# Kernel optimization log

Measured on AMD Instinct MI355X. Metric: run time of the kernel, lower is better.

The kernel has to match this reference:

```python
import jax, jax.numpy as jnp
import numpy as np

B, N, C = 4, 2048, 1024
H = 16
D = C // H

def setup_inputs() -> dict:
    key = jax.random.key(0)
    k1, k2, k3 = jax.random.split(key, 3)
    x = jax.random.normal(k1, (B, N, C), dtype=jnp.float32)
    qkv_w = jax.random.normal(k2, (3 * C, C), dtype=jnp.float32) * (1.0 / np.sqrt(C))
    qkv_b = jax.random.normal(k3, (3 * C,), dtype=jnp.float32) * 0.02
    return {"x": x, "qkv_w": qkv_w, "qkv_b": qkv_b}

def reference(x, qkv_w, qkv_b):
    b, n, c = x.shape
    # torch Linear: x @ W^T + b
    qkv = x @ qkv_w.T + qkv_b                      # [B,N,3C]
    qkv = qkv.reshape(b, n, 3, H, D)
    qkv = jnp.transpose(qkv, (2, 0, 3, 1, 4))       # [3,B,H,N,D]
    q, k, v = qkv[0], qkv[1], qkv[2]
    attn = jnp.einsum('bhnd,bhmd->bhnm', q, k) / jnp.sqrt(jnp.asarray(D, x.dtype))
    attn = jax.nn.softmax(attn, axis=-1)
    out = jnp.einsum('bhnm,bhmd->bhnd', attn, v)    # [B,H,N,D]
    out = jnp.transpose(out, (0, 2, 1, 3)).reshape(b, n, c)
    return out
```

## Files before the change

kernel.cpp:

```cpp
#include <hip/hip_runtime.h>
#include <hip/hip_bf16.h>

typedef __attribute__((ext_vector_type(8))) short short8;
typedef __attribute__((ext_vector_type(4))) float f32x4;
typedef __attribute__((ext_vector_type(4))) unsigned int u32x4;
typedef unsigned short u16;
typedef unsigned int u32;

typedef u32 __attribute__((address_space(1))) as1_u32;
typedef u32 __attribute__((address_space(3))) as3_u32;

#define NB 4
#define SEQ 2048
#define CH 1024
#define NH 16
#define HD 64
#define M_TOT (NB*SEQ)
#define N_TOT (3*CH)
#define K_TOT CH
#define SCL 0.18033688f

#define MFMA16(a,b,c) __builtin_amdgcn_mfma_f32_16x16x32_bf16((a),(b),(c),0,0,0)

__device__ __forceinline__ u16 f2bf(float f) {
    union { float f; u32 u; } v; v.f = f;
    u32 u = v.u;
    return (u16)((u + 0x7fffu + ((u >> 16) & 1u)) >> 16);
}

__device__ __forceinline__ u32 pkbf2(float a, float b) {
    union { __hip_bfloat162 h; u32 u; } x;
    x.h = __float22bfloat162_rn(float2{a, b});
    return x.u;
}

__global__ void cvt_bf16_kernel(const float* __restrict__ src, u16* __restrict__ dst, int n8) {
    int i = blockIdx.x * 256 + threadIdx.x;
    if (i >= n8) return;
    const float4* s4 = (const float4*)src;
    float4 a = s4[2*i], b = s4[2*i+1];
    u32x4 r;
    r[0] = pkbf2(a.x, a.y); r[1] = pkbf2(a.z, a.w);
    r[2] = pkbf2(b.x, b.y); r[3] = pkbf2(b.z, b.w);
    *(u32x4*)(dst + (size_t)i*8) = r;
}

__global__ __launch_bounds__(256) void qkv_gemm_kernel(
        const u16* __restrict__ A, const u16* __restrict__ W,
        const float* __restrict__ bias,
        u16* __restrict__ qw, u16* __restrict__ kw, u16* __restrict__ vtw)
{
    __shared__ u16 As[128*32];
    __shared__ u16 Bs[128*32];
    const int t = threadIdx.x;
    const int wave = t >> 6;
    const int lane = t & 63;
    const int l15 = lane & 15, lhi = lane >> 4;
    const int wr = wave >> 1, wc = wave & 1;
    const int bm = blockIdx.x, bn = blockIdx.y;

    f32x4 acc[4][4] = {};

    const int arow = t >> 2;
    const int acol = (t & 3) * 8;
    const u16* gA = A + (size_t)(bm*128 + arow)*K_TOT + acol;
    const u16* gB = W + (size_t)(bn*128 + arow)*K_TOT + acol;

    for (int k0 = 0; k0 < K_TOT; k0 += 32) {
        #pragma unroll
        for (int i = 0; i < 2; ++i) {
            __builtin_amdgcn_global_load_lds(
                (const as1_u32*)(gA + (size_t)i*64*K_TOT + k0),
                (as3_u32*)(As + i*2048 + wave*512), 16, 0, 0);
            __builtin_amdgcn_global_load_lds(
                (const as1_u32*)(gB + (size_t)i*64*K_TOT + k0),
                (as3_u32*)(Bs + i*2048 + wave*512), 16, 0, 0);
        }
        __syncthreads();
        short8 af[4], bfr[4];
        #pragma unroll
        for (int m = 0; m < 4; ++m)
            af[m] = *(const short8*)(As + (wr*64 + m*16 + l15)*32 + lhi*8);
        #pragma unroll
        for (int n = 0; n < 4; ++n)
            bfr[n] = *(const short8*)(Bs + (wc*64 + n*16 + l15)*32 + lhi*8);
        #pragma unroll
        for (int m = 0; m < 4; ++m)
            #pragma unroll
            for (int n = 0; n < 4; ++n)
                acc[m][n] = MFMA16(af[m], bfr[n], acc[m][n]);
        __syncthreads();
    }

    const int colbase = bn*128 + wc*64;
    const int which = colbase >> 10;
    float bv[4]; int hh[4], dd[4];
    #pragma unroll
    for (int n = 0; n < 4; ++n) {
        int cg = colbase + n*16 + l15;
        bv[n] = bias[cg];
        int hd = cg & 1023;
        hh[n] = hd >> 6; dd[n] = hd & 63;
    }
    #pragma unroll
    for (int m = 0; m < 4; ++m) {
        int rowg = bm*128 + wr*64 + m*16 + lhi*4;
        #pragma unroll
        for (int j = 0; j < 4; ++j) {
            int rg = rowg + j;
            int b = rg >> 11, nseq = rg & 2047;
            #pragma unroll
            for (int n = 0; n < 4; ++n) {
                float val = acc[m][n][j] + bv[n];
                size_t bhn = (size_t)(b*NH + hh[n]);
                if (which == 0) {
                    qw[(bhn*SEQ + nseq)*HD + dd[n]] = f2bf(val * SCL);
                } else if (which == 1) {
                    kw[(bhn*SEQ + nseq)*HD + dd[n]] = f2bf(val);
                } else {
                    vtw[(bhn*HD + dd[n])*SEQ + nseq] = f2bf(val);
                }
            }
        }
    }
}

__global__ __launch_bounds__(512, 4) void attn_kernel(
        const u16* __restrict__ qw, const u16* __restrict__ kw,
        const u16* __restrict__ vtw, float* __restrict__ out)
{
    __shared__ u16 Ksh[2][64*64];
    __shared__ u16 Vsh[2][64*64];
    const int t = threadIdx.x;
    const int wave = t >> 6, lane = t & 63;
    const int l15 = lane & 15, lhi = lane >> 4;
    const int bh = blockIdx.y;
    const int b = bh >> 4, h = bh & 15;
    const int q0 = blockIdx.x * 256 + wave * 32;

    const u16* Q  = qw  + (size_t)bh * SEQ * HD;
    const u16* Kg = kw  + (size_t)bh * SEQ * HD;
    const u16* Vg = vtw + (size_t)bh * HD * SEQ;

    const int srow = lane >> 3;
    const int scol = ((lane & 7) ^ srow) * 8;
    const int crow = wave * 8 + srow;
    const int kperm = (crow & 32) | ((crow & 12) << 1)
                    | ((crow & 16) >> 2) | (crow & 3);

    auto STAGE = [&](int buf, int kv) {
        __builtin_amdgcn_global_load_lds(
            (const as1_u32*)(Kg + (size_t)(kv + kperm)*HD + scol),
            (as3_u32*)(&Ksh[buf][wave*8*64]), 16, 0, 0);
        __builtin_amdgcn_global_load_lds(
            (const as1_u32*)(Vg + (size_t)crow*SEQ + kv + scol),
            (as3_u32*)(&Vsh[buf][wave*8*64]), 16, 0, 0);
    };

    STAGE(0, 0);

    short8 qf[2][2];
    #pragma unroll
    for (int rf = 0; rf < 2; ++rf)
        #pragma unroll
        for (int ks = 0; ks < 2; ++ks)
            qf[rf][ks] = *(const short8*)(Q + (size_t)(q0 + rf*16 + l15)*HD + ks*32 + lhi*8);

    f32x4 o[2][4] = {};
    float lpart[2] = {0.f, 0.f};

    __syncthreads();

    int cur = 0;
    for (int kv0 = 0; kv0 < SEQ; kv0 += 64) {
        if (kv0 + 64 < SEQ) STAGE(cur ^ 1, kv0 + 64);

        f32x4 st[2][4] = {};
        #pragma unroll
        for (int g = 0; g < 4; ++g)
            #pragma unroll
            for (int ks = 0; ks < 2; ++ks) {
                short8 kf = *(const short8*)(&Ksh[cur][(g*16 + l15)*64 + ((ks*32 + lhi*8) ^ ((l15 & 7)*8))]);
                st[0][g] = MFMA16(kf, qf[0][ks], st[0][g]);
                st[1][g] = MFMA16(kf, qf[1][ks], st[1][g]);
            }

        u32x4 pa[2][2];
        #pragma unroll
        for (int rf = 0; rf < 2; ++rf)
            #pragma unroll
            for (int g = 0; g < 4; ++g) {
                float p0 = __builtin_amdgcn_exp2f(st[rf][g][0]);
                float p1 = __builtin_amdgcn_exp2f(st[rf][g][1]);
                float p2 = __builtin_amdgcn_exp2f(st[rf][g][2]);
                float p3 = __builtin_amdgcn_exp2f(st[rf][g][3]);
                lpart[rf] += (p0 + p1) + (p2 + p3);
                pa[rf][g >> 1][(g & 1)*2]     = pkbf2(p0, p1);
                pa[rf][g >> 1][(g & 1)*2 + 1] = pkbf2(p2, p3);
            }

        #pragma unroll
        for (int ks = 0; ks < 2; ++ks) {
            short8 pa0 = __builtin_bit_cast(short8, pa[0][ks]);
            short8 pa1 = __builtin_bit_cast(short8, pa[1][ks]);
            #pragma unroll
            for (int nd = 0; nd < 4; ++nd) {
                short8 vf = *(const short8*)(&Vsh[cur][(nd*16 + l15)*64 + ((ks*32 + lhi*8) ^ ((l15 & 7)*8))]);
                o[0][nd] = MFMA16(pa0, vf, o[0][nd]);
                o[1][nd] = MFMA16(pa1, vf, o[1][nd]);
            }
        }
        __syncthreads();
        cur ^= 1;
    }

    #pragma unroll
    for (int rf = 0; rf < 2; ++rf) {
        float l = lpart[rf];
        l += __shfl_xor(l, 16);
        l += __shfl_xor(l, 32);
        #pragma unroll
        for (int j = 0; j < 4; ++j) {
            float inv = 1.0f / __shfl(l, lhi*4 + j);
            int qrow = q0 + rf*16 + lhi*4 + j;
            float* orow = out + ((size_t)(b*SEQ + qrow))*CH + h*HD;
            #pragma unroll
            for (int nd = 0; nd < 4; ++nd)
                orow[nd*16 + l15] = o[rf][nd][j] * inv;
        }
    }
}

extern "C" void kernel_launch(void* const* d_in, const int* in_sizes, int n_in,
                              void* d_out, int out_size, void* d_ws, size_t ws_size,
                              hipStream_t stream) {
    const float* x    = (const float*)d_in[0];
    const float* w    = (const float*)d_in[1];
    const float* bias = (const float*)d_in[2];
    float* out = (float*)d_out;

    const size_t BHND = (size_t)NB*NH*SEQ*HD;
    u16* qw  = (u16*)d_ws;
    u16* kw  = qw  + BHND;
    u16* vtw = kw  + BHND;
    u16* xbf = vtw + BHND;
    u16* wbf = xbf + (size_t)M_TOT*K_TOT;

    int nx8 = M_TOT*K_TOT/8;
    int nw8 = N_TOT*K_TOT/8;
    cvt_bf16_kernel<<<nx8/256, 256, 0, stream>>>(x, xbf, nx8);
    cvt_bf16_kernel<<<nw8/256, 256, 0, stream>>>(w, wbf, nw8);
    qkv_gemm_kernel<<<dim3(M_TOT/128, N_TOT/128), 256, 0, stream>>>(xbf, wbf, bias, qw, kw, vtw);
    attn_kernel<<<dim3(SEQ/256, NB*NH), 512, 0, stream>>>(qw, kw, vtw, out);
}
```

Measured before the change: 176.1 us.

## Triple-buffer attention K/V, remap block order, fuse bf16 conversion launches

The two fp32-to-bf16 conversion launches are merged into one. The QKV GEMM grid is flattened and its blocks reordered across groups of eight, apparently for better L2 locality across XCDs. The attention kernel switches from double to triple buffering: a manual vmcnt wait plus a single barrier per tile replaces the two syncthreads, and s_setprio raises wave priority around the MFMA sections. This adds LDS per block, which may reduce occupancy, and the correctness of the hand-written wait counts depends on how the compiler orders instructions.

```diff
diff --git a/kernel.cpp b/kernel.cpp
--- a/kernel.cpp
+++ b/kernel.cpp
@@ -34,15 +34,18 @@
     return x.u;
 }
 
-__global__ void cvt_bf16_kernel(const float* __restrict__ src, u16* __restrict__ dst, int n8) {
+__global__ void cvt_bf16_kernel(const float* __restrict__ x, u16* __restrict__ xb, int nx8,
+                                const float* __restrict__ w, u16* __restrict__ wb, int nw8) {
     int i = blockIdx.x * 256 + threadIdx.x;
-    if (i >= n8) return;
+    const float* src; u16* dst; int idx;
+    if (i < nx8) { src = x; dst = xb; idx = i; }
+    else { idx = i - nx8; if (idx >= nw8) return; src = w; dst = wb; }
     const float4* s4 = (const float4*)src;
-    float4 a = s4[2*i], b = s4[2*i+1];
+    float4 a = s4[2*idx], b = s4[2*idx+1];
     u32x4 r;
     r[0] = pkbf2(a.x, a.y); r[1] = pkbf2(a.z, a.w);
     r[2] = pkbf2(b.x, b.y); r[3] = pkbf2(b.z, b.w);
-    *(u32x4*)(dst + (size_t)i*8) = r;
+    *(u32x4*)(dst + (size_t)idx*8) = r;
 }
 
 __global__ __launch_bounds__(256) void qkv_gemm_kernel(
@@ -57,7 +60,8 @@
     const int lane = t & 63;
     const int l15 = lane & 15, lhi = lane >> 4;
     const int wr = wave >> 1, wc = wave & 1;
-    const int bm = blockIdx.x, bn = blockIdx.y;
+    const int s = (blockIdx.x & 7) * 192 + (blockIdx.x >> 3);
+    const int bm = s & 63, bn = s >> 6;
 
     f32x4 acc[4][4] = {};
 
@@ -129,14 +133,14 @@
         const u16* __restrict__ qw, const u16* __restrict__ kw,
         const u16* __restrict__ vtw, float* __restrict__ out)
 {
-    __shared__ u16 Ksh[2][64*64];
-    __shared__ u16 Vsh[2][64*64];
+    __shared__ u16 Ksh[3][64*64];
+    __shared__ u16 Vsh[3][64*64];
     const int t = threadIdx.x;
     const int wave = t >> 6, lane = t & 63;
     const int l15 = lane & 15, lhi = lane >> 4;
-    const int bh = blockIdx.y;
+    const int bh = blockIdx.x & 63;
     const int b = bh >> 4, h = bh & 15;
-    const int q0 = blockIdx.x * 256 + wave * 32;
+    const int q0 = (blockIdx.x >> 6) * 256 + wave * 32;
 
     const u16* Q  = qw  + (size_t)bh * SEQ * HD;
     const u16* Kg = kw  + (size_t)bh * SEQ * HD;
@@ -158,6 +162,7 @@
     };
 
     STAGE(0, 0);
+    STAGE(1, 64);
 
     short8 qf[2][2];
     #pragma unroll
@@ -169,13 +174,19 @@
     f32x4 o[2][4] = {};
     float lpart[2] = {0.f, 0.f};
 
-    __syncthreads();
-
+    const int NT = SEQ / 64;
     int cur = 0;
-    for (int kv0 = 0; kv0 < SEQ; kv0 += 64) {
-        if (kv0 + 64 < SEQ) STAGE(cur ^ 1, kv0 + 64);
+    for (int tt = 0; tt < NT; ++tt) {
+        asm volatile("s_waitcnt vmcnt(2)" ::: "memory");
+        __builtin_amdgcn_s_barrier();
+        __builtin_amdgcn_sched_barrier(0);
+
+        int nxt = cur + 2; if (nxt >= 3) nxt -= 3;
+        int kvn = (tt + 2 < NT) ? (tt + 2) * 64 : 0;
+        STAGE(nxt, kvn);
 
         f32x4 st[2][4] = {};
+        __builtin_amdgcn_s_setprio(1);
         #pragma unroll
         for (int g = 0; g < 4; ++g)
             #pragma unroll
@@ -184,6 +195,7 @@
                 st[0][g] = MFMA16(kf, qf[0][ks], st[0][g]);
                 st[1][g] = MFMA16(kf, qf[1][ks], st[1][g]);
             }
+        __builtin_amdgcn_s_setprio(0);
 
         u32x4 pa[2][2];
         #pragma unroll
@@ -199,6 +211,7 @@
                 pa[rf][g >> 1][(g & 1)*2 + 1] = pkbf2(p2, p3);
             }
 
+        __builtin_amdgcn_s_setprio(1);
         #pragma unroll
         for (int ks = 0; ks < 2; ++ks) {
             short8 pa0 = __builtin_bit_cast(short8, pa[0][ks]);
@@ -210,8 +223,9 @@
                 o[1][nd] = MFMA16(pa1, vf, o[1][nd]);
             }
         }
-        __syncthreads();
-        cur ^= 1;
+        __builtin_amdgcn_s_setprio(0);
+
+        cur = cur + 1; if (cur >= 3) cur -= 3;
     }
 
     #pragma unroll
@@ -246,10 +260,9 @@
     u16* xbf = vtw + BHND;
     u16* wbf = xbf + (size_t)M_TOT*K_TOT;
 
-    int nx8 = M_TOT*K_TOT/8;
-    int nw8 = N_TOT*K_TOT/8;
-    cvt_bf16_kernel<<<nx8/256, 256, 0, stream>>>(x, xbf, nx8);
-    cvt_bf16_kernel<<<nw8/256, 256, 0, stream>>>(w, wbf, nw8);
-    qkv_gemm_kernel<<<dim3(M_TOT/128, N_TOT/128), 256, 0, stream>>>(xbf, wbf, bias, qw, kw, vtw);
-    attn_kernel<<<dim3(SEQ/256, NB*NH), 512, 0, stream>>>(qw, kw, vtw, out);
-}
+    const int nx8 = M_TOT*K_TOT/8;
+    const int nw8 = N_TOT*K_TOT/8;
+    cvt_bf16_kernel<<<(nx8+nw8+255)/256, 256, 0, stream>>>(x, xbf, nx8, w, wbf, nw8);
+    qkv_gemm_kernel<<<(M_TOT/128)*(N_TOT/128), 256, 0, stream>>>(xbf, wbf, bias, qw, kw, vtw);
+    attn_kernel<<<(SEQ/256)*NB*NH, 512, 0, stream>>>(qw, kw, vtw, out);
+}
```

Measured after the change: 196.0 us. 1.11x slower.
